# Kernel optimization log

Hardware: AMD Instinct MI355X
Metric: run time of the kernel (lower is better)

## Reference

```python
import jax, jax.numpy as jnp
import numpy as np

B, NQ, NK, D, H = 4, 1024, 1024, 1024, 16
HD = D // H
SCALE = HD ** -0.5
LN_EPS = 1e-5


def setup_inputs() -> dict:
    key = jax.random.key(0)
    ks = jax.random.split(key, 16)
    s = 0.02
    inp = {
        "query": jax.random.normal(ks[0], (B, NQ, D), jnp.float32),
        "key": jax.random.normal(ks[1], (B, NK, D), jnp.float32),
        "value": jax.random.normal(ks[2], (B, NK, D), jnp.float32),
        # attention projections (torch Linear: [out, in] weights)
        "wq": jax.random.normal(ks[3], (D, D), jnp.float32) * s,
        "bq": jnp.zeros((D,), jnp.float32),
        "wk": jax.random.normal(ks[4], (D, D), jnp.float32) * s,
        "bk": jnp.zeros((D,), jnp.float32),
        "wv": jax.random.normal(ks[5], (D, D), jnp.float32) * s,
        "bv": jnp.zeros((D,), jnp.float32),
        "wo": jax.random.normal(ks[6], (D, D), jnp.float32) * s,
        "bo": jnp.zeros((D,), jnp.float32),
        # vad_proj: Linear(D, D//2) -> GELU -> Linear(D//2, 3) -> Tanh
        "w1": jax.random.normal(ks[7], (D // 2, D), jnp.float32) * s,
        "b1": jnp.zeros((D // 2,), jnp.float32),
        "w2": jax.random.normal(ks[8], (3, D // 2), jnp.float32) * s,
        "b2": jnp.zeros((3,), jnp.float32),
        "vad_lambda": jnp.asarray(0.1, jnp.float32),
        "ln_g": jnp.ones((D,), jnp.float32),
        "ln_b": jnp.zeros((D,), jnp.float32),
    }
    return inp


def _vad(x, w1, b1, w2, b2):
    h = jax.nn.gelu(x @ w1.T + b1, approximate=False)
    return jnp.tanh(h @ w2.T + b2)  # [B, N, 3]


def _layer_norm(x, g, b):
    mu = jnp.mean(x, axis=-1, keepdims=True)
    var = jnp.mean(jnp.square(x - mu), axis=-1, keepdims=True)
    return (x - mu) * jax.lax.rsqrt(var + LN_EPS) * g + b


def reference(query, key, value, wq, bq, wk, bk, wv, bv, wo, bo,
              w1, b1, w2, b2, vad_lambda, ln_g, ln_b):
    Bq, Nq, Dm = query.shape
    Nk = key.shape[1]
    # project and split heads: [B, H, N, HD]
    Q = (query @ wq.T + bq).reshape(Bq, Nq, H, HD).transpose(0, 2, 1, 3)
    K = (key @ wk.T + bk).reshape(Bq, Nk, H, HD).transpose(0, 2, 1, 3)
    V = (value @ wv.T + bv).reshape(Bq, Nk, H, HD).transpose(0, 2, 1, 3)
    scores = jnp.einsum("bhqd,bhkd->bhqk", Q, K) * SCALE  # [B,H,Nq,Nk]
    # VAD affinity: -||v_q[i] - v_k[j]||_2
    vq = _vad(query, w1, b1, w2, b2)  # [B,Nq,3]
    vk = _vad(key, w1, b1, w2, b2)    # [B,Nk,3]
    diff = vq[:, :, None, :] - vk[:, None, :, :]         # [B,Nq,Nk,3]
    affinity = -jnp.sqrt(jnp.sum(diff * diff, axis=-1))  # [B,Nq,Nk]
    guided = scores + vad_lambda * affinity[:, None, :, :]
    attn = jax.nn.softmax(guided, axis=-1)
    out = jnp.einsum("bhqk,bhkd->bhqd", attn, V)
    out = out.transpose(0, 2, 1, 3).reshape(Bq, Nq, Dm)
    out = out @ wo.T + bo
    return _layer_norm(query + out, ln_g, ln_b)
```

## Files before the change

### kernel.cpp

```cpp
#include <hip/hip_runtime.h>
#include <hip/hip_bf16.h>

typedef float f32x4 __attribute__((ext_vector_type(4)));
typedef float f32x16 __attribute__((ext_vector_type(16)));
typedef __bf16 bf16x8 __attribute__((ext_vector_type(8)));
typedef unsigned short us8 __attribute__((ext_vector_type(8)));
typedef unsigned short us4 __attribute__((ext_vector_type(4)));

#define DEVI __device__ __forceinline__
#define LOG2E 1.44269504088896f

DEVI unsigned short f2bf(float x) {
  return __builtin_bit_cast(unsigned short, __float2bfloat16(x));
}
DEVI float bf2f(unsigned short u) {
  return __builtin_bit_cast(float, ((unsigned int)u) << 16);
}
DEVI bf16x8 ldb8(const unsigned short* p) {
  return __builtin_bit_cast(bf16x8, *(const us8*)p);
}
DEVI void gload16(const unsigned short* g, unsigned short* l) {
  __builtin_amdgcn_global_load_lds(
      (const __attribute__((address_space(1))) unsigned int*)(const void*)g,
      (__attribute__((address_space(3))) unsigned int*)(void*)l, 16, 0, 0);
}

__global__ __launch_bounds__(256) void cvt3_k(const float* __restrict__ p0, const float* __restrict__ p1,
                                              const float* __restrict__ p2,
                                              unsigned short* __restrict__ o0, unsigned short* __restrict__ o1,
                                              unsigned short* __restrict__ o2, int n) {
  const float* in;
  unsigned short* out;
  switch (blockIdx.y) {
    case 0: in = p0; out = o0; break;
    case 1: in = p1; out = o1; break;
    default: in = p2; out = o2; break;
  }
  int i = (blockIdx.x * 256 + threadIdx.x) * 8;
  if (i >= n) return;
  float4 a = *(const float4*)(in + i);
  float4 b = *(const float4*)(in + i + 4);
  us8 r = {f2bf(a.x), f2bf(a.y), f2bf(a.z), f2bf(a.w), f2bf(b.x), f2bf(b.y), f2bf(b.z), f2bf(b.w)};
  *(us8*)(out + i) = r;
}

__global__ __launch_bounds__(256) void cvt5_k(const float* __restrict__ p0, const float* __restrict__ p1,
                                              const float* __restrict__ p2, const float* __restrict__ p3,
                                              const float* __restrict__ p4,
                                              unsigned short* __restrict__ o0, unsigned short* __restrict__ o1,
                                              unsigned short* __restrict__ o2, unsigned short* __restrict__ o3,
                                              unsigned short* __restrict__ o4) {
  const float* in;
  unsigned short* out;
  int n = 1048576;
  switch (blockIdx.y) {
    case 0: in = p0; out = o0; break;
    case 1: in = p1; out = o1; break;
    case 2: in = p2; out = o2; break;
    case 3: in = p3; out = o3; break;
    default: in = p4; out = o4; n = 524288; break;
  }
  int i = (blockIdx.x * 256 + threadIdx.x) * 8;
  if (i >= n) return;
  float4 a = *(const float4*)(in + i);
  float4 b = *(const float4*)(in + i + 4);
  us8 r = {f2bf(a.x), f2bf(a.y), f2bf(a.z), f2bf(a.w), f2bf(b.x), f2bf(b.y), f2bf(b.z), f2bf(b.w)};
  *(us8*)(out + i) = r;
}

template <int EPI>
DEVI void gemm_body(const unsigned short* __restrict__ A, const unsigned short* __restrict__ W,
                    const float* __restrict__ bias, void* __restrict__ Cout,
                    int N, int K, int lda, float oscale, int brow, int bcol,
                    unsigned short* As, unsigned short* Bs, int t) {
  const int l = t & 63;
  const int w4 = t >> 6, wr = w4 >> 1, wc = w4 & 1;
  const int l5 = l & 31, hi = l >> 5;
  f32x16 acc[2][2] = {};
  for (int kt = 0; kt < K; kt += 64) {
    __syncthreads();
#pragma unroll
    for (int i = 0; i < 4; ++i) {
      int c = t + i * 256;
      int row = c >> 3;
      int sw = (((c & 7) ^ (row & 7) ^ ((row >> 3) & 3))) * 8;
      gload16(A + (size_t)(brow + row) * lda + kt + sw, As + c * 8);
      gload16(W + (size_t)(bcol + row) * lda + kt + sw, Bs + c * 8);
    }
    __syncthreads();
#pragma unroll
    for (int ks = 0; ks < 4; ++ks) {
      bf16x8 af[2], bfr[2];
      const int ch = (ks * 2 + hi) ^ (l5 & 7) ^ ((l5 >> 3) & 3);
#pragma unroll
      for (int mi = 0; mi < 2; ++mi)
        af[mi] = ldb8(&As[(wr * 64 + mi * 32 + l5) * 64 + ch * 8]);
#pragma unroll
      for (int ni = 0; ni < 2; ++ni)
        bfr[ni] = ldb8(&Bs[(wc * 64 + ni * 32 + l5) * 64 + ch * 8]);
#pragma unroll
      for (int mi = 0; mi < 2; ++mi)
#pragma unroll
        for (int ni = 0; ni < 2; ++ni)
          acc[mi][ni] = __builtin_amdgcn_mfma_f32_32x32x16_bf16(af[mi], bfr[ni], acc[mi][ni], 0, 0, 0);
    }
  }
#pragma unroll
  for (int mi = 0; mi < 2; ++mi)
#pragma unroll
    for (int ni = 0; ni < 2; ++ni) {
      int col = bcol + wc * 64 + ni * 32 + l5;
      int rowBase = brow + wr * 64 + mi * 32 + hi * 4;
      float bc = (EPI == 3) ? 0.f : bias[col];
#pragma unroll
      for (int reg = 0; reg < 16; ++reg) {
        int row = rowBase + (reg & 3) + 8 * (reg >> 2);
        float v;
        if (EPI == 3)
          v = (acc[mi][ni][reg] + bias[row]) * oscale;
        else if (EPI == 2)
          v = acc[mi][ni][reg] + 0.5f * bc;
        else
          v = (acc[mi][ni][reg] + bc) * oscale;
        if (EPI == 1) v = 0.5f * v * (1.0f + erff(v * 0.70710678118f));
        ((unsigned short*)Cout)[(size_t)row * N + col] = f2bf(v);
      }
    }
}

__global__ __launch_bounds__(256) void proj_k(const unsigned short* __restrict__ qb, const unsigned short* __restrict__ kb,
                                              const unsigned short* __restrict__ vb,
                                              const unsigned short* __restrict__ wqb, const unsigned short* __restrict__ wkb,
                                              const unsigned short* __restrict__ wvb, const unsigned short* __restrict__ w1b,
                                              const float* __restrict__ bq, const float* __restrict__ bk,
                                              const float* __restrict__ bv, const float* __restrict__ b1,
                                              unsigned short* __restrict__ Qp, unsigned short* __restrict__ Kp,
                                              unsigned short* __restrict__ Vt,
                                              unsigned short* __restrict__ h1q, unsigned short* __restrict__ h1k) {
  __shared__ unsigned short As[8192];
  __shared__ unsigned short Bs[8192];
  const int t = threadIdx.x;
  const int lin = blockIdx.x;
  const int nl = (lin & 7) * 128 + (lin >> 3);
  if (nl < 256) {
    gemm_body<0>(qb, wqb, bq, Qp, 1024, 1024, 1024, 0.125f * LOG2E,
                 (nl >> 3) * 128, (nl & 7) * 128, As, Bs, t);
  } else if (nl < 512) {
    int s = nl - 256;
    gemm_body<0>(kb, wkb, bk, Kp, 1024, 1024, 1024, 1.f,
                 (s >> 3) * 128, (s & 7) * 128, As, Bs, t);
  } else if (nl < 768) {
    int s = nl - 512;
    gemm_body<3>(wvb, vb, bv, Vt, 4096, 1024, 1024, 1.f,
                 (s >> 5) * 128, (s & 31) * 128, As, Bs, t);
  } else {
    int s = nl - 768;
    const unsigned short* A = (s >= 128) ? kb : qb;
    unsigned short* C = (s >= 128) ? h1k : h1q;
    int s2 = s & 127;
    gemm_body<1>(A, w1b, b1, C, 512, 1024, 1024, 1.f,
                 (s2 >> 2) * 128, (s2 & 3) * 128, As, Bs, t);
  }
}

__global__ __launch_bounds__(256) void wo_k(const unsigned short* __restrict__ Obuf, const unsigned short* __restrict__ wob,
                                            const float* __restrict__ bo,
                                            unsigned short* __restrict__ tmpA, unsigned short* __restrict__ tmpB) {
  __shared__ unsigned short As[8192];
  __shared__ unsigned short Bs[8192];
  const int t = threadIdx.x;
  const int lin = blockIdx.x;
  const int nl = (lin & 7) * 64 + (lin >> 3);
  const int z = nl >> 8, s = nl & 255;
  gemm_body<2>(Obuf + z * 512, wob + z * 512, bo, z ? tmpB : tmpA,
               1024, 512, 1024, 1.f, (s >> 3) * 128, (s & 7) * 128, As, Bs, t);
}

__global__ __launch_bounds__(256) void vad2_k(const unsigned short* __restrict__ h1a, const unsigned short* __restrict__ h1b,
                                              const float* __restrict__ w2, const float* __restrict__ b2,
                                              float* __restrict__ outa, float* __restrict__ outb) {
  const unsigned short* h1 = blockIdx.y ? h1b : h1a;
  float* out = blockIdx.y ? outb : outa;
  const int t = threadIdx.x, l = t & 63, w = t >> 6;
  const int row = blockIdx.x * 4 + w;
  us8 hv = *(const us8*)(h1 + (size_t)row * 512 + l * 8);
  float hf[8];
#pragma unroll
  for (int j = 0; j < 8; ++j) hf[j] = bf2f(hv[j]);
  float s[3];
#pragma unroll
  for (int c = 0; c < 3; ++c) {
    const float* wp = w2 + c * 512 + l * 8;
    float a = 0.f;
#pragma unroll
    for (int j = 0; j < 8; ++j) a += hf[j] * wp[j];
    s[c] = a;
  }
#pragma unroll
  for (int m = 1; m < 64; m <<= 1) {
#pragma unroll
    for (int c = 0; c < 3; ++c) s[c] += __shfl_xor(s[c], m, 64);
  }
  if (l == 0) {
#pragma unroll
    for (int c = 0; c < 3; ++c) out[(size_t)row * 3 + c] = tanhf(s[c] + b2[c]);
  }
}

__global__ __launch_bounds__(256) void aff_k(const float* __restrict__ vq, const float* __restrict__ vk,
                                             const float* __restrict__ plam, unsigned short* __restrict__ aff) {
  __shared__ float vqs[64][3], vks[64][3];
  const int t = threadIdx.x;
  const int b = blockIdx.z, q0 = blockIdx.y * 64, k0 = blockIdx.x * 64;
  const float lam2 = plam[0] * LOG2E;
  if (t < 192) {
    ((float*)vqs)[t] = vq[((size_t)b * 1024 + q0) * 3 + t];
    ((float*)vks)[t] = vk[((size_t)b * 1024 + k0) * 3 + t];
  }
  __syncthreads();
  const int q = t >> 2, kc = (t & 3) * 16;
  const float a0 = vqs[q][0], a1 = vqs[q][1], a2 = vqs[q][2];
  unsigned short o[16];
#pragma unroll
  for (int j = 0; j < 16; ++j) {
    int k = kc + j;
    float dx = a0 - vks[k][0], dy = a1 - vks[k][1], dz = a2 - vks[k][2];
    o[j] = f2bf(-lam2 * sqrtf(dx * dx + dy * dy + dz * dz));
  }
  unsigned short* dst = aff + ((size_t)(b * 1024 + q0 + q)) * 1024 + k0 + kc;
  *(us8*)dst = *(us8*)&o[0];
  *(us8*)(dst + 8) = *(us8*)&o[8];
}

__global__ __launch_bounds__(512, 2) void attn_k(const unsigned short* __restrict__ Qp,
                                                 const unsigned short* __restrict__ Kp,
                                                 const unsigned short* __restrict__ Vt,
                                                 const unsigned short* __restrict__ aff,
                                                 unsigned short* __restrict__ Obuf) {
  __shared__ unsigned short Ks[2][4096];
  __shared__ unsigned short Vs[2][4096];
  __shared__ unsigned short Ps[8][1024];
  const int lin = blockIdx.x + 8 * (blockIdx.y + 16 * blockIdx.z);
  const int nl = (lin & 7) * 64 + (lin >> 3);
  const int qb = nl & 7, h = (nl >> 3) & 15, b = nl >> 7;
  const int t = threadIdx.x, l = t & 63, w = t >> 6;
  const int l4 = l & 15, lg = l >> 4;
  const size_t qrow0 = (size_t)b * 1024 + qb * 128;
  const int hoff = h * 64;

  bf16x8 qf[2];
#pragma unroll
  for (int ks = 0; ks < 2; ++ks)
    qf[ks] = ldb8(Qp + (qrow0 + w * 16 + l4) * 1024 + hoff + ks * 32 + lg * 8);

  {
    const unsigned short* gk = Kp + ((size_t)b * 1024) * 1024 + hoff;
    const unsigned short* gv = Vt + (size_t)hoff * 4096 + (size_t)b * 1024;
    int c = t, row = c >> 3, sw = ((c & 7) ^ (row & 7)) * 8;
    gload16(gk + (size_t)row * 1024 + sw, Ks[0] + c * 8);
    gload16(gv + (size_t)row * 4096 + sw, Vs[0] + c * 8);
  }
  float l_run = 0.f;
  f32x4 accO[4] = {};
  const unsigned short* ab = aff + (qrow0 + w * 16 + l4) * 1024 + lg * 4;
  __syncthreads();

  int cur = 0;
  for (int kt = 0; kt < 16; ++kt) {
    if (kt < 15) {
      const unsigned short* gk = Kp + ((size_t)b * 1024 + (kt + 1) * 64) * 1024 + hoff;
      const unsigned short* gv = Vt + (size_t)hoff * 4096 + (size_t)b * 1024 + (kt + 1) * 64;
      int c = t, row = c >> 3, sw = ((c & 7) ^ (row & 7)) * 8;
      gload16(gk + (size_t)row * 1024 + sw, Ks[cur ^ 1] + c * 8);
      gload16(gv + (size_t)row * 4096 + sw, Vs[cur ^ 1] + c * 8);
    }
    f32x4 sc[4];
#pragma unroll
    for (int jt = 0; jt < 4; ++jt) {
      us4 av = *(const us4*)(ab + kt * 64 + jt * 16);
#pragma unroll
      for (int r = 0; r < 4; ++r) sc[jt][r] = bf2f(av[r]);
    }
    __builtin_amdgcn_s_setprio(1);
#pragma unroll
    for (int jt = 0; jt < 4; ++jt) {
#pragma unroll
      for (int ks = 0; ks < 2; ++ks) {
        bf16x8 kf = ldb8(&Ks[cur][(jt * 16 + l4) * 64 + (((ks * 4 + lg) ^ (l4 & 7))) * 8]);
        sc[jt] = __builtin_amdgcn_mfma_f32_16x16x32_bf16(kf, qf[ks], sc[jt], 0, 0, 0);
      }
    }
    __builtin_amdgcn_s_setprio(0);
    float pv[4][4];
    float rs = 0.f;
#pragma unroll
    for (int jt = 0; jt < 4; ++jt)
#pragma unroll
      for (int r = 0; r < 4; ++r) { pv[jt][r] = exp2f(sc[jt][r]); rs += pv[jt][r]; }
    l_run += rs;
    char* pw = (char*)&Ps[w][0];
#pragma unroll
    for (int jt = 0; jt < 4; ++jt) {
      unsigned int p0, p1;
      asm("v_cvt_pk_bf16_f32 %0, %1, %2" : "=v"(p0) : "v"(pv[jt][0]), "v"(pv[jt][1]));
      asm("v_cvt_pk_bf16_f32 %0, %1, %2" : "=v"(p1) : "v"(pv[jt][2]), "v"(pv[jt][3]));
      int chunk = (jt * 2 + (lg >> 1)) ^ (l4 & 7);
      *(unsigned long long*)(pw + l4 * 128 + chunk * 16 + (lg & 1) * 8) =
          (unsigned long long)p0 | ((unsigned long long)p1 << 32);
    }
    __builtin_amdgcn_s_setprio(1);
#pragma unroll
    for (int js = 0; js < 2; ++js) {
      bf16x8 pa = ldb8(&Ps[w][l4 * 64 + (((js * 4 + lg) ^ (l4 & 7))) * 8]);
#pragma unroll
      for (int dt = 0; dt < 4; ++dt) {
        bf16x8 vf = ldb8(&Vs[cur][(dt * 16 + l4) * 64 + (((js * 4 + lg) ^ (l4 & 7))) * 8]);
        accO[dt] = __builtin_amdgcn_mfma_f32_16x16x32_bf16(pa, vf, accO[dt], 0, 0, 0);
      }
    }
    __builtin_amdgcn_s_setprio(0);
    __syncthreads();
    cur ^= 1;
  }
  l_run += __shfl_xor(l_run, 16, 64);
  l_run += __shfl_xor(l_run, 32, 64);
  float linv = 1.f / l_run;
  float lr[4];
#pragma unroll
  for (int r = 0; r < 4; ++r) lr[r] = __shfl(linv, lg * 4 + r, 16);
#pragma unroll
  for (int dt = 0; dt < 4; ++dt)
#pragma unroll
    for (int r = 0; r < 4; ++r) {
      float v = accO[dt][r] * lr[r];
      Obuf[(qrow0 + w * 16 + lg * 4 + r) * 1024 + hoff + dt * 16 + l4] = f2bf(v);
    }
}

__global__ __launch_bounds__(256) void ln_k(const float* __restrict__ q,
                                            const unsigned short* __restrict__ ta,
                                            const unsigned short* __restrict__ tb,
                                            const float* __restrict__ g,
                                            const float* __restrict__ bb,
                                            float* __restrict__ out) {
  __shared__ float red[8];
  const int row = blockIdx.x, t = threadIdx.x;
  const int l = t & 63, w = t >> 6;
  const size_t base = (size_t)row * 1024 + t * 4;
  float4 a = *(const float4*)(q + base);
  us4 cv = *(const us4*)(ta + base);
  us4 dv = *(const us4*)(tb + base);
  float x0 = a.x + bf2f(cv[0]) + bf2f(dv[0]);
  float x1 = a.y + bf2f(cv[1]) + bf2f(dv[1]);
  float x2 = a.z + bf2f(cv[2]) + bf2f(dv[2]);
  float x3 = a.w + bf2f(cv[3]) + bf2f(dv[3]);
  float s = x0 + x1 + x2 + x3;
#pragma unroll
  for (int m = 1; m < 64; m <<= 1) s += __shfl_xor(s, m, 64);
  if (l == 0) red[w] = s;
  __syncthreads();
  float mean = (red[0] + red[1] + red[2] + red[3]) * (1.f / 1024.f);
  float d0 = x0 - mean, d1 = x1 - mean, d2 = x2 - mean, d3 = x3 - mean;
  float v = d0 * d0 + d1 * d1 + d2 * d2 + d3 * d3;
#pragma unroll
  for (int m = 1; m < 64; m <<= 1) v += __shfl_xor(v, m, 64);
  if (l == 0) red[4 + w] = v;
  __syncthreads();
  float var = (red[4] + red[5] + red[6] + red[7]) * (1.f / 1024.f);
  float rstd = rsqrtf(var + 1e-5f);
  float4 gv = *(const float4*)(g + t * 4);
  float4 bv = *(const float4*)(bb + t * 4);
  float4 o;
  o.x = d0 * rstd * gv.x + bv.x;
  o.y = d1 * rstd * gv.y + bv.y;
  o.z = d2 * rstd * gv.z + bv.z;
  o.w = d3 * rstd * gv.w + bv.w;
  *(float4*)(out + (size_t)row * 1024 + t * 4) = o;
}

extern "C" void kernel_launch(void* const* d_in, const int* in_sizes, int n_in,
                              void* d_out, int out_size, void* d_ws, size_t ws_size,
                              hipStream_t stream) {
  const float* query = (const float*)d_in[0];
  const float* key_  = (const float*)d_in[1];
  const float* value = (const float*)d_in[2];
  const float* wq = (const float*)d_in[3];
  const float* bq = (const float*)d_in[4];
  const float* wk = (const float*)d_in[5];
  const float* bk = (const float*)d_in[6];
  const float* wv = (const float*)d_in[7];
  const float* bv = (const float*)d_in[8];
  const float* wo = (const float*)d_in[9];
  const float* bo = (const float*)d_in[10];
  const float* w1 = (const float*)d_in[11];
  const float* b1 = (const float*)d_in[12];
  const float* w2 = (const float*)d_in[13];
  const float* b2 = (const float*)d_in[14];
  const float* lam = (const float*)d_in[15];
  const float* lng = (const float*)d_in[16];
  const float* lnb = (const float*)d_in[17];

  char* ws = (char*)d_ws;
  size_t off = 0;
  auto alloc = [&](size_t n) { char* p = ws + off; off += (n + 255) & ~(size_t)255; return p; };
  unsigned short* qb  = (unsigned short*)alloc(8388608);
  unsigned short* kb  = (unsigned short*)alloc(8388608);
  unsigned short* vb  = (unsigned short*)alloc(8388608);
  unsigned short* wqb = (unsigned short*)alloc(2097152);
  unsigned short* wkb = (unsigned short*)alloc(2097152);
  unsigned short* wvb = (unsigned short*)alloc(2097152);
  unsigned short* wob = (unsigned short*)alloc(2097152);
  unsigned short* w1b = (unsigned short*)alloc(1048576);
  unsigned short* Qp  = (unsigned short*)alloc(8388608);
  unsigned short* Kp  = (unsigned short*)alloc(8388608);
  unsigned short* Vt  = (unsigned short*)alloc(8388608);
  unsigned short* h1q = (unsigned short*)alloc(4194304);
  unsigned short* h1k = (unsigned short*)alloc(4194304);
  float* vadq = (float*)alloc(49152);
  float* vadk = (float*)alloc(49152);
  unsigned short* Obuf = (unsigned short*)alloc(8388608);
  unsigned short* aff  = vb;
  unsigned short* tmpA = qb;
  unsigned short* tmpB = kb;

  cvt3_k<<<dim3(2048, 3), 256, 0, stream>>>(query, key_, value, qb, kb, vb, 4194304);
  cvt5_k<<<dim3(512, 5), 256, 0, stream>>>(wq, wk, wv, wo, w1, wqb, wkb, wvb, wob, w1b);

  proj_k<<<1024, 256, 0, stream>>>(qb, kb, vb, wqb, wkb, wvb, w1b,
                                   bq, bk, bv, b1, Qp, Kp, Vt, h1q, h1k);
  vad2_k<<<dim3(1024, 2), 256, 0, stream>>>(h1q, h1k, w2, b2, vadq, vadk);
  aff_k<<<dim3(16, 16, 4), 256, 0, stream>>>(vadq, vadk, lam, aff);
  attn_k<<<dim3(8, 16, 4), 512, 0, stream>>>(Qp, Kp, Vt, aff, Obuf);
  wo_k<<<512, 256, 0, stream>>>(Obuf, wob, bo, tmpA, tmpB);
  ln_k<<<4096, 256, 0, stream>>>(query, tmpA, tmpB, lng, lnb, (float*)d_out);
}
```

Before: 154.8 us.

## Fuse VAD second linear into W1 GEMM epilogue with atomic partial sums

The W1 GEMM epilogue now applies GELU, stages the tile in shared memory, and dot-products each row with w2. It atomically accumulates the three partial outputs into a zeroed buffer, and tanh plus bias moves into the affinity kernel. This removes the h1 intermediate write and read and the separate vad2 kernel, at the cost of a small zeroing launch and float atomics with non-deterministic summation order. The attention kernel's launch bounds minimum-blocks hint also rises from 2 to 6, which pushes register allocation down.

```diff
diff --git a/kernel.cpp b/kernel.cpp
--- a/kernel.cpp
+++ b/kernel.cpp
@@ -68,11 +68,18 @@
   *(us8*)(out + i) = r;
 }
 
+__global__ __launch_bounds__(256) void zero_k(float* __restrict__ a, float* __restrict__ b) {
+  int i = blockIdx.x * 256 + threadIdx.x;
+  if (i < 3072) ((float4*)a)[i] = float4{0.f, 0.f, 0.f, 0.f};
+  else ((float4*)b)[i - 3072] = float4{0.f, 0.f, 0.f, 0.f};
+}
+
 template <int EPI>
 DEVI void gemm_body(const unsigned short* __restrict__ A, const unsigned short* __restrict__ W,
                     const float* __restrict__ bias, void* __restrict__ Cout,
                     int N, int K, int lda, float oscale, int brow, int bcol,
-                    unsigned short* As, unsigned short* Bs, int t) {
+                    unsigned short* As, unsigned short* Bs, int t,
+                    const float* __restrict__ w2) {
   const int l = t & 63;
   const int w4 = t >> 6, wr = w4 >> 1, wc = w4 & 1;
   const int l5 = l & 31, hi = l >> 5;
@@ -104,6 +111,51 @@
         for (int ni = 0; ni < 2; ++ni)
           acc[mi][ni] = __builtin_amdgcn_mfma_f32_32x32x16_bf16(af[mi], bfr[ni], acc[mi][ni], 0, 0, 0);
     }
+  }
+  if (EPI == 1) {
+    __syncthreads();
+    unsigned short* half = wc ? Bs : As;
+#pragma unroll
+    for (int mi = 0; mi < 2; ++mi)
+#pragma unroll
+      for (int ni = 0; ni < 2; ++ni) {
+        int colL = ni * 32 + l5;
+        float bc = bias[bcol + wc * 64 + colL];
+#pragma unroll
+        for (int reg = 0; reg < 16; ++reg) {
+          int rowL = wr * 64 + mi * 32 + hi * 4 + (reg & 3) + 8 * (reg >> 2);
+          float v = acc[mi][ni][reg] + bc;
+          v = 0.5f * v * (1.0f + erff(v * 0.70710678118f));
+          half[rowL * 64 + colL] = f2bf(v);
+        }
+      }
+    __syncthreads();
+    const int row = t >> 1, ch2 = t & 1;
+    const unsigned short* src = ch2 ? Bs : As;
+    const float* w2c = w2 + bcol + ch2 * 64;
+    float s0 = 0.f, s1 = 0.f, s2 = 0.f;
+#pragma unroll
+    for (int jq = 0; jq < 8; ++jq) {
+      us8 gv = *(const us8*)(src + row * 64 + jq * 8);
+#pragma unroll
+      for (int j = 0; j < 8; ++j) {
+        float g = bf2f(gv[j]);
+        int col = jq * 8 + j;
+        s0 += g * w2c[col];
+        s1 += g * w2c[512 + col];
+        s2 += g * w2c[1024 + col];
+      }
+    }
+    s0 += __shfl_xor(s0, 1, 64);
+    s1 += __shfl_xor(s1, 1, 64);
+    s2 += __shfl_xor(s2, 1, 64);
+    if (!ch2) {
+      float* vp = (float*)Cout + (size_t)(brow + row) * 3;
+      atomicAdd(vp, s0);
+      atomicAdd(vp + 1, s1);
+      atomicAdd(vp + 2, s2);
+    }
+    return;
   }
 #pragma unroll
   for (int mi = 0; mi < 2; ++mi)
@@ -122,7 +174,6 @@
           v = acc[mi][ni][reg] + 0.5f * bc;
         else
           v = (acc[mi][ni][reg] + bc) * oscale;
-        if (EPI == 1) v = 0.5f * v * (1.0f + erff(v * 0.70710678118f));
         ((unsigned short*)Cout)[(size_t)row * N + col] = f2bf(v);
       }
     }
@@ -134,9 +185,10 @@
                                               const unsigned short* __restrict__ wvb, const unsigned short* __restrict__ w1b,
                                               const float* __restrict__ bq, const float* __restrict__ bk,
                                               const float* __restrict__ bv, const float* __restrict__ b1,
+                                              const float* __restrict__ w2,
                                               unsigned short* __restrict__ Qp, unsigned short* __restrict__ Kp,
                                               unsigned short* __restrict__ Vt,
-                                              unsigned short* __restrict__ h1q, unsigned short* __restrict__ h1k) {
+                                              float* __restrict__ vadq, float* __restrict__ vadk) {
   __shared__ unsigned short As[8192];
   __shared__ unsigned short Bs[8192];
   const int t = threadIdx.x;
@@ -144,22 +196,22 @@
   const int nl = (lin & 7) * 128 + (lin >> 3);
   if (nl < 256) {
     gemm_body<0>(qb, wqb, bq, Qp, 1024, 1024, 1024, 0.125f * LOG2E,
-                 (nl >> 3) * 128, (nl & 7) * 128, As, Bs, t);
+                 (nl >> 3) * 128, (nl & 7) * 128, As, Bs, t, nullptr);
   } else if (nl < 512) {
     int s = nl - 256;
     gemm_body<0>(kb, wkb, bk, Kp, 1024, 1024, 1024, 1.f,
-                 (s >> 3) * 128, (s & 7) * 128, As, Bs, t);
+                 (s >> 3) * 128, (s & 7) * 128, As, Bs, t, nullptr);
   } else if (nl < 768) {
     int s = nl - 512;
     gemm_body<3>(wvb, vb, bv, Vt, 4096, 1024, 1024, 1.f,
-                 (s >> 5) * 128, (s & 31) * 128, As, Bs, t);
+                 (s >> 5) * 128, (s & 31) * 128, As, Bs, t, nullptr);
   } else {
     int s = nl - 768;
     const unsigned short* A = (s >= 128) ? kb : qb;
-    unsigned short* C = (s >= 128) ? h1k : h1q;
+    float* V = (s >= 128) ? vadk : vadq;
     int s2 = s & 127;
-    gemm_body<1>(A, w1b, b1, C, 512, 1024, 1024, 1.f,
-                 (s2 >> 2) * 128, (s2 & 3) * 128, As, Bs, t);
+    gemm_body<1>(A, w1b, b1, V, 512, 1024, 1024, 1.f,
+                 (s2 >> 2) * 128, (s2 & 3) * 128, As, Bs, t, w2);
   }
 }
 
@@ -173,49 +225,20 @@
   const int nl = (lin & 7) * 64 + (lin >> 3);
   const int z = nl >> 8, s = nl & 255;
   gemm_body<2>(Obuf + z * 512, wob + z * 512, bo, z ? tmpB : tmpA,
-               1024, 512, 1024, 1.f, (s >> 3) * 128, (s & 7) * 128, As, Bs, t);
-}
-
-__global__ __launch_bounds__(256) void vad2_k(const unsigned short* __restrict__ h1a, const unsigned short* __restrict__ h1b,
-                                              const float* __restrict__ w2, const float* __restrict__ b2,
-                                              float* __restrict__ outa, float* __restrict__ outb) {
-  const unsigned short* h1 = blockIdx.y ? h1b : h1a;
-  float* out = blockIdx.y ? outb : outa;
-  const int t = threadIdx.x, l = t & 63, w = t >> 6;
-  const int row = blockIdx.x * 4 + w;
-  us8 hv = *(const us8*)(h1 + (size_t)row * 512 + l * 8);
-  float hf[8];
-#pragma unroll
-  for (int j = 0; j < 8; ++j) hf[j] = bf2f(hv[j]);
-  float s[3];
-#pragma unroll
-  for (int c = 0; c < 3; ++c) {
-    const float* wp = w2 + c * 512 + l * 8;
-    float a = 0.f;
-#pragma unroll
-    for (int j = 0; j < 8; ++j) a += hf[j] * wp[j];
-    s[c] = a;
-  }
-#pragma unroll
-  for (int m = 1; m < 64; m <<= 1) {
-#pragma unroll
-    for (int c = 0; c < 3; ++c) s[c] += __shfl_xor(s[c], m, 64);
-  }
-  if (l == 0) {
-#pragma unroll
-    for (int c = 0; c < 3; ++c) out[(size_t)row * 3 + c] = tanhf(s[c] + b2[c]);
-  }
+               1024, 512, 1024, 1.f, (s >> 3) * 128, (s & 7) * 128, As, Bs, t, nullptr);
 }
 
 __global__ __launch_bounds__(256) void aff_k(const float* __restrict__ vq, const float* __restrict__ vk,
-                                             const float* __restrict__ plam, unsigned short* __restrict__ aff) {
+                                             const float* __restrict__ plam, const float* __restrict__ b2,
+                                             unsigned short* __restrict__ aff) {
   __shared__ float vqs[64][3], vks[64][3];
   const int t = threadIdx.x;
   const int b = blockIdx.z, q0 = blockIdx.y * 64, k0 = blockIdx.x * 64;
   const float lam2 = plam[0] * LOG2E;
   if (t < 192) {
-    ((float*)vqs)[t] = vq[((size_t)b * 1024 + q0) * 3 + t];
-    ((float*)vks)[t] = vk[((size_t)b * 1024 + k0) * 3 + t];
+    float bb = b2[t % 3];
+    ((float*)vqs)[t] = tanhf(vq[((size_t)b * 1024 + q0) * 3 + t] + bb);
+    ((float*)vks)[t] = tanhf(vk[((size_t)b * 1024 + k0) * 3 + t] + bb);
   }
   __syncthreads();
   const int q = t >> 2, kc = (t & 3) * 16;
@@ -232,7 +255,7 @@
   *(us8*)(dst + 8) = *(us8*)&o[8];
 }
 
-__global__ __launch_bounds__(512, 2) void attn_k(const unsigned short* __restrict__ Qp,
+__global__ __launch_bounds__(512, 6) void attn_k(const unsigned short* __restrict__ Qp,
                                                  const unsigned short* __restrict__ Kp,
                                                  const unsigned short* __restrict__ Vt,
                                                  const unsigned short* __restrict__ aff,
@@ -414,8 +437,6 @@
   unsigned short* Qp  = (unsigned short*)alloc(8388608);
   unsigned short* Kp  = (unsigned short*)alloc(8388608);
   unsigned short* Vt  = (unsigned short*)alloc(8388608);
-  unsigned short* h1q = (unsigned short*)alloc(4194304);
-  unsigned short* h1k = (unsigned short*)alloc(4194304);
   float* vadq = (float*)alloc(49152);
   float* vadk = (float*)alloc(49152);
   unsigned short* Obuf = (unsigned short*)alloc(8388608);
@@ -425,11 +446,11 @@
 
   cvt3_k<<<dim3(2048, 3), 256, 0, stream>>>(query, key_, value, qb, kb, vb, 4194304);
   cvt5_k<<<dim3(512, 5), 256, 0, stream>>>(wq, wk, wv, wo, w1, wqb, wkb, wvb, wob, w1b);
+  zero_k<<<24, 256, 0, stream>>>(vadq, vadk);
 
   proj_k<<<1024, 256, 0, stream>>>(qb, kb, vb, wqb, wkb, wvb, w1b,
-                                   bq, bk, bv, b1, Qp, Kp, Vt, h1q, h1k);
-  vad2_k<<<dim3(1024, 2), 256, 0, stream>>>(h1q, h1k, w2, b2, vadq, vadk);
-  aff_k<<<dim3(16, 16, 4), 256, 0, stream>>>(vadq, vadk, lam, aff);
+                                   bq, bk, bv, b1, w2, Qp, Kp, Vt, vadq, vadk);
+  aff_k<<<dim3(16, 16, 4), 256, 0, stream>>>(vadq, vadk, lam, b2, aff);
   attn_k<<<dim3(8, 16, 4), 512, 0, stream>>>(Qp, Kp, Vt, aff, Obuf);
   wo_k<<<512, 256, 0, stream>>>(Obuf, wob, bo, tmpA, tmpB);
   ln_k<<<4096, 256, 0, stream>>>(query, tmpA, tmpB, lng, lnb, (float*)d_out);
```

Measured after the change: 158.3 us. +2.2%, slower.
